# Performance work log

Hardware: AMD Instinct MI355X
Metric: run time of the kernel (lower is better)

## Reference

```python
import jax, jax.numpy as jnp
import numpy as np

B, S, E = 4, 2048, 1024


def setup_inputs() -> dict:
    key = jax.random.key(0)
    k1, k2, k3, k4 = jax.random.split(key, 4)
    scale = 1.0 / np.sqrt(E)
    return {
        "x": jax.random.normal(k1, (B, S, E), dtype=jnp.float32),
        "W_Q": jax.random.normal(k2, (E, E), dtype=jnp.float32) * scale,
        "W_K": jax.random.normal(k3, (E, E), dtype=jnp.float32) * scale,
        "W_V": jax.random.normal(k4, (E, E), dtype=jnp.float32) * scale,
    }


def reference(x, W_Q, W_K, W_V):
    # nn.Linear(E, E, bias=False): y = x @ W.T
    Q = jnp.einsum("bse,fe->bsf", x, W_Q)
    K = jnp.einsum("bse,fe->bsf", x, W_K)
    V = jnp.einsum("bse,fe->bsf", x, W_V)
    d = Q.shape[-1]
    scores = jnp.einsum("bqd,bkd->bqk", Q, K) / jnp.sqrt(jnp.float32(d))
    # causal mask: -inf strictly above the diagonal
    seq = Q.shape[1]
    causal = jnp.tril(jnp.ones((seq, seq), dtype=bool))  # [S,S]
    scores = jnp.where(causal[None, :, :], scores, jnp.float32(-jnp.inf))
    attn = jax.nn.softmax(scores, axis=-1)
    return jnp.einsum("bqk,bkd->bqd", attn, V)
```

## Files before the change

kernel.cpp:

```cpp
#include <hip/hip_runtime.h>
#include <hip/hip_bf16.h>
#include <stdint.h>

typedef __hip_bfloat16 bf16;
typedef __attribute__((ext_vector_type(8))) short bf16x8;
typedef __attribute__((ext_vector_type(4))) float f32x4;
typedef __attribute__((ext_vector_type(8))) unsigned short u16x8;
typedef __attribute__((ext_vector_type(4))) unsigned short u16x4;

#define SLEN 2048
#define ED   1024
#define NB   4
#define AS1 __attribute__((address_space(1)))
#define AS3 __attribute__((address_space(3)))
#define SB0() __builtin_amdgcn_sched_barrier(0)

static __device__ __forceinline__ unsigned short f2bf(float f) {
    return __builtin_bit_cast(unsigned short, __float2bfloat16(f));
}

__device__ __forceinline__ void gemm8p(
    const char* __restrict__ aT, int lda,
    const char* __restrict__ bT, int ldb,
    int nkt, char* sm, int tid, f32x4 (&acc)[8][4])
{
    const int lane = tid & 63, wave = tid >> 6;
    const int wm = wave >> 2, wn = wave & 3;
    const int fr = lane & 15, kc = lane >> 4;

    auto SU = [&](int isB, int kh, int Tn) {
        char* dst = sm + (Tn & 1) * 65536 + isB * 32768 + kh * 16384;
        const char* g = isB ? bT : aT;
        const int ld = isB ? ldb : lda;
#pragma unroll
        for (int j = 0; j < 2; ++j) {
            int rid = j * 512 + tid;
            int row = rid >> 2, c = rid & 3;
            const char* src = g + (size_t)row * ld + Tn * 128 + kh * 64
                            + ((c ^ ((row >> 1) & 3)) * 16);
            __builtin_amdgcn_global_load_lds(
                (const AS1 uint32_t*)src,
                (AS3 uint32_t*)(dst + (j * 512 + wave * 64) * 16), 16, 0, 0);
        }
    };
    auto RDA = [&](int T, int kh, bf16x8 (&a)[8]) {
        const char* pa = sm + (T & 1) * 65536 + kh * 16384;
#pragma unroll
        for (int i = 0; i < 8; ++i) {
            int row = wm * 128 + i * 16 + fr;
            a[i] = *(const bf16x8*)(pa + row * 64 + ((kc ^ ((row >> 1) & 3)) * 16));
        }
    };
    auto RDB = [&](int T, int kh, int nh, bf16x8 (&b)[2]) {
        const char* pb = sm + (T & 1) * 65536 + 32768 + kh * 16384;
#pragma unroll
        for (int n = 0; n < 2; ++n) {
            int row = wn * 64 + nh * 32 + n * 16 + fr;
            b[n] = *(const bf16x8*)(pb + row * 64 + ((kc ^ ((row >> 1) & 3)) * 16));
        }
    };
    auto MM = [&](bf16x8 (&a)[8], bf16x8 (&b)[2], int nh) {
        __builtin_amdgcn_s_setprio(1);
#pragma unroll
        for (int i = 0; i < 8; ++i)
#pragma unroll
            for (int n = 0; n < 2; ++n)
                acc[i][nh * 2 + n] = __builtin_amdgcn_mfma_f32_16x16x32_bf16(
                    a[i], b[n], acc[i][nh * 2 + n], 0, 0, 0);
        __builtin_amdgcn_s_setprio(0);
    };

    SU(0, 0, 0); SU(1, 0, 0); SU(0, 1, 0); SU(1, 1, 0);
    SU(0, 0, 1); SU(1, 0, 1); SU(0, 1, 1);
    asm volatile("s_waitcnt vmcnt(6)" ::: "memory");
    SB0();
    __builtin_amdgcn_s_barrier();

    for (int T = 0; T < nkt; ++T) {
        const bool p1 = (T + 1 < nkt), p2 = (T + 2 < nkt);
        bf16x8 a[8], b[2];
        RDA(T, 0, a); RDB(T, 0, 0, b);
        if (p1) SU(1, 1, T + 1);
        SB0(); __builtin_amdgcn_s_barrier();
        asm volatile("s_waitcnt lgkmcnt(0)" ::: "memory");
        SB0();
        MM(a, b, 0);
        SB0(); __builtin_amdgcn_s_barrier();
        RDB(T, 0, 1, b);
        if (p2) SU(0, 0, T + 2);
        SB0(); __builtin_amdgcn_s_barrier();
        asm volatile("s_waitcnt lgkmcnt(0)" ::: "memory");
        SB0();
        MM(a, b, 1);
        SB0(); __builtin_amdgcn_s_barrier();
        RDA(T, 1, a); RDB(T, 1, 0, b);
        if (p2) SU(1, 0, T + 2);
        SB0(); __builtin_amdgcn_s_barrier();
        asm volatile("s_waitcnt lgkmcnt(0)" ::: "memory");
        SB0();
        MM(a, b, 0);
        SB0(); __builtin_amdgcn_s_barrier();
        RDB(T, 1, 1, b);
        if (p2) SU(0, 1, T + 2);
        if (T < nkt - 2) asm volatile("s_waitcnt vmcnt(6)" ::: "memory");
        else             asm volatile("s_waitcnt vmcnt(0)" ::: "memory");
        SB0(); __builtin_amdgcn_s_barrier();
        asm volatile("s_waitcnt lgkmcnt(0)" ::: "memory");
        SB0();
        MM(a, b, 1);
        SB0(); __builtin_amdgcn_s_barrier();
    }
}

__device__ __forceinline__ void gemm_core8(
    const char* __restrict__ aT, int lda,
    const char* __restrict__ bT, int ldb,
    int nkt, char* sm, int tid, f32x4 (&acc)[4][4])
{
    const int lane = tid & 63, wave = tid >> 6;
    const int wm = wave >> 1, wn = wave & 1;
    const int fr = lane & 15, kc = lane >> 4;

    auto STAGE = [&](int kh, int Tn) {
        char* buf = sm + (Tn & 1) * 49152;
#pragma unroll
        for (int j = 0; j < 2; ++j) {
            int rid = j * 512 + tid;
            int row = rid >> 2, c = rid & 3;
            const char* src = aT + (size_t)row * lda + Tn * 128 + kh * 64
                            + ((c ^ ((row >> 1) & 3)) * 16);
            __builtin_amdgcn_global_load_lds(
                (const AS1 uint32_t*)src,
                (AS3 uint32_t*)(buf + kh * 16384 + (j * 512 + wave * 64) * 16),
                16, 0, 0);
        }
        {
            int row = tid >> 2, c = tid & 3;
            const char* src = bT + (size_t)row * ldb + Tn * 128 + kh * 64
                            + ((c ^ ((row >> 1) & 3)) * 16);
            __builtin_amdgcn_global_load_lds(
                (const AS1 uint32_t*)src,
                (AS3 uint32_t*)(buf + 32768 + kh * 8192 + (wave * 64) * 16),
                16, 0, 0);
        }
    };
    auto RD = [&](int T, int kh, bf16x8 (&a)[4], bf16x8 (&b)[4]) {
        const char* buf = sm + (T & 1) * 49152;
#pragma unroll
        for (int i = 0; i < 4; ++i) {
            int row = wm * 64 + i * 16 + fr;
            a[i] = *(const bf16x8*)(buf + kh * 16384 + row * 64
                                    + ((kc ^ ((row >> 1) & 3)) * 16));
        }
#pragma unroll
        for (int i = 0; i < 4; ++i) {
            int row = wn * 64 + i * 16 + fr;
            b[i] = *(const bf16x8*)(buf + 32768 + kh * 8192 + row * 64
                                    + ((kc ^ ((row >> 1) & 3)) * 16));
        }
    };
    auto MM = [&](bf16x8 (&a)[4], bf16x8 (&b)[4]) {
        __builtin_amdgcn_s_setprio(1);
#pragma unroll
        for (int i = 0; i < 4; ++i)
#pragma unroll
            for (int n = 0; n < 4; ++n)
                acc[i][n] = __builtin_amdgcn_mfma_f32_16x16x32_bf16(
                    a[i], b[n], acc[i][n], 0, 0, 0);
        __builtin_amdgcn_s_setprio(0);
    };

    STAGE(0, 0); STAGE(1, 0);
    asm volatile("s_waitcnt vmcnt(3)" ::: "memory");
    SB0();
    __builtin_amdgcn_s_barrier();

    bf16x8 aE[4], bE[4], aO[4], bO[4];
    for (int T = 0; T < nkt; ++T) {
        const bool pre = (T + 1 < nkt);
        RD(T, 0, aE, bE);
        SB0();
        if (pre) STAGE(0, T + 1);
        SB0();
        if (T > 0) {
            asm volatile("s_waitcnt lgkmcnt(8)" ::: "memory");
            SB0();
            MM(aO, bO);
        }
        if (pre) asm volatile("s_waitcnt vmcnt(3)" ::: "memory");
        else     asm volatile("s_waitcnt vmcnt(0)" ::: "memory");
        SB0();
        __builtin_amdgcn_s_barrier();
        RD(T, 1, aO, bO);
        SB0();
        if (pre) STAGE(1, T + 1);
        SB0();
        asm volatile("s_waitcnt lgkmcnt(8)" ::: "memory");
        SB0();
        MM(aE, bE);
        if (pre) asm volatile("s_waitcnt vmcnt(3)" ::: "memory");
        else     asm volatile("s_waitcnt vmcnt(0)" ::: "memory");
        SB0();
        __builtin_amdgcn_s_barrier();
    }
    asm volatile("s_waitcnt lgkmcnt(0)" ::: "memory");
    SB0();
    MM(aO, bO);
}

__global__ __launch_bounds__(256) void convert_to_bf16(
    const float* __restrict__ x, const float* __restrict__ wq,
    const float* __restrict__ wk, const float* __restrict__ wv,
    bf16* __restrict__ xb, bf16* __restrict__ wqb,
    bf16* __restrict__ wkb, bf16* __restrict__ wvb)
{
    long g = (long)blockIdx.x * 256 + threadIdx.x;
    const float* src; bf16* dst; long o;
    if (g < 1048576) { src = x; dst = xb; o = g * 8; }
    else {
        long g2 = g - 1048576;
        int w = (int)(g2 >> 17);
        o = (g2 & 131071) * 8;
        src = (w == 0) ? wq : (w == 1) ? wk : wv;
        dst = (w == 0) ? wqb : (w == 1) ? wkb : wvb;
    }
    float4 v0 = *(const float4*)(src + o);
    float4 v1 = *(const float4*)(src + o + 4);
    u16x8 r;
    r[0] = f2bf(v0.x); r[1] = f2bf(v0.y); r[2] = f2bf(v0.z); r[3] = f2bf(v0.w);
    r[4] = f2bf(v1.x); r[5] = f2bf(v1.y); r[6] = f2bf(v1.z); r[7] = f2bf(v1.w);
    *(u16x8*)(dst + o) = r;
}

__global__ __launch_bounds__(512, 2) void qkv_gemm(
    const bf16* __restrict__ xb, const bf16* __restrict__ wqb,
    const bf16* __restrict__ wkb, const bf16* __restrict__ wvb,
    bf16* __restrict__ Qb, bf16* __restrict__ Kb, bf16* __restrict__ Vt)
{
    extern __shared__ char smem[];
    int bid = blockIdx.x, tid = threadIdx.x;
    int xcd = bid & 7, i = bid >> 3;
    int tm = (xcd << 2) | (i & 3);
    int tn = i >> 2;
    const bf16* W = (tn < 8) ? wqb : (tn < 16) ? wkb : wvb;
    int tnl = tn & 7;
    f32x4 acc[4][4] = {};
    gemm_core8((const char*)(xb + (size_t)tm * 256 * ED), ED * 2,
               (const char*)(W + (size_t)tnl * 128 * ED), ED * 2,
               16, smem, tid, acc);

    int lane = tid & 63, wave = tid >> 6, wm = wave >> 1, wn = wave & 1;
    int rl = (lane >> 4) * 4, cl = lane & 15;
    if (tn < 16) {
        bf16* C = (tn < 8) ? Qb : Kb;
#pragma unroll
        for (int mf = 0; mf < 4; ++mf)
#pragma unroll
            for (int j = 0; j < 4; ++j) {
                int r = tm * 256 + wm * 64 + mf * 16 + rl + j;
#pragma unroll
                for (int nf = 0; nf < 4; ++nf) {
                    int c = tnl * 128 + wn * 64 + nf * 16 + cl;
                    C[(size_t)r * ED + c] = __float2bfloat16(acc[mf][nf][j]);
                }
            }
    } else {
#pragma unroll
        for (int mf = 0; mf < 4; ++mf)
#pragma unroll
            for (int j = 0; j < 4; ++j) {
                int r = tm * 256 + wm * 64 + mf * 16 + rl + j;
                int bb = r >> 11, s = r & 2047;
#pragma unroll
                for (int nf = 0; nf < 4; ++nf) {
                    int d = tnl * 128 + wn * 64 + nf * 16 + cl;
                    Vt[(((size_t)bb << 10) + d) * SLEN + s] = __float2bfloat16(acc[mf][nf][j]);
                }
            }
    }
}

__global__ __launch_bounds__(512, 2) void qk_gemm(
    const bf16* __restrict__ Qb, const bf16* __restrict__ Kb, float* __restrict__ Sc)
{
    extern __shared__ char smem[];
    int t = blockIdx.x, b = blockIdx.y, tid = threadIdx.x;
    int ti = 0;
    while ((ti + 1) * (ti + 2) / 2 <= t) ++ti;
    int tj = t - ti * (ti + 1) / 2;
    f32x4 acc[8][4] = {};
    gemm8p((const char*)(Qb + ((size_t)b * SLEN + ti * 256) * ED), ED * 2,
           (const char*)(Kb + ((size_t)b * SLEN + tj * 256) * ED), ED * 2,
           16, smem, tid, acc);

    float* Sb = Sc + (size_t)b * SLEN * SLEN;
    int lane = tid & 63, wave = tid >> 6, wm = wave >> 2, wn = wave & 3;
    int rl = (lane >> 4) * 4, cl = lane & 15;
#pragma unroll
    for (int mf = 0; mf < 8; ++mf)
#pragma unroll
        for (int j = 0; j < 4; ++j) {
            int r = ti * 256 + wm * 128 + mf * 16 + rl + j;
#pragma unroll
            for (int nf = 0; nf < 4; ++nf) {
                int c = tj * 256 + wn * 64 + nf * 16 + cl;
                Sb[(size_t)r * SLEN + c] = acc[mf][nf][j] * 0.03125f;
            }
        }
}

__global__ __launch_bounds__(256) void softmax_rows(float* __restrict__ Sc)
{
    int q = blockIdx.x, b = blockIdx.y, tid = threadIdx.x;
    float* row = Sc + ((size_t)b * SLEN + q) * SLEN;
    int lane = tid & 63, wave = tid >> 6;
    __shared__ float red[4];

    float vals[8];
    float lmax = -3.0e38f;
#pragma unroll
    for (int r = 0; r < 2; ++r) {
        int i4 = tid + r * 256;
        if (i4 * 4 <= q) {
            float4 v = *(const float4*)(row + i4 * 4);
            vals[r * 4 + 0] = v.x; vals[r * 4 + 1] = v.y;
            vals[r * 4 + 2] = v.z; vals[r * 4 + 3] = v.w;
#pragma unroll
            for (int e = 0; e < 4; ++e) {
                int k = i4 * 4 + e;
                if (k <= q) lmax = fmaxf(lmax, vals[r * 4 + e]);
            }
        }
    }
#pragma unroll
    for (int o = 32; o > 0; o >>= 1) lmax = fmaxf(lmax, __shfl_xor(lmax, o));
    if (lane == 0) red[wave] = lmax;
    __syncthreads();
    float m = fmaxf(fmaxf(red[0], red[1]), fmaxf(red[2], red[3]));
    __syncthreads();
    float lsum = 0.f;
#pragma unroll
    for (int r = 0; r < 2; ++r) {
        int i4 = tid + r * 256;
        if (i4 * 4 <= q)
#pragma unroll
            for (int e = 0; e < 4; ++e) {
                int k = i4 * 4 + e;
                if (k <= q) lsum += __expf(vals[r * 4 + e] - m);
            }
    }
#pragma unroll
    for (int o = 32; o > 0; o >>= 1) lsum += __shfl_xor(lsum, o);
    if (lane == 0) red[wave] = lsum;
    __syncthreads();
    float inv = 1.0f / (red[0] + red[1] + red[2] + red[3]);
    unsigned short* prow = (unsigned short*)row;
    int kmax = ((q >> 8) + 1) << 8;
#pragma unroll
    for (int r = 0; r < 2; ++r) {
        int i4 = tid + r * 256;
        if (i4 * 4 < kmax) {
            u16x4 o4;
#pragma unroll
            for (int e = 0; e < 4; ++e) {
                int k = i4 * 4 + e;
                float p = (k <= q) ? __expf(vals[r * 4 + e] - m) * inv : 0.0f;
                o4[e] = f2bf(p);
            }
            *(u16x4*)(prow + i4 * 4) = o4;
        }
    }
}

__global__ __launch_bounds__(512, 2) void pv_gemm(
    const bf16* __restrict__ P, const bf16* __restrict__ Vt, float* __restrict__ O)
{
    extern __shared__ char smem[];
    int mq = 7 - blockIdx.x, nd = blockIdx.y, b = blockIdx.z, tid = threadIdx.x;
    f32x4 acc[4][4] = {};
    int nkt = (mq + 1) * 4;
    gemm_core8((const char*)P + ((size_t)b * SLEN + mq * 256) * 8192, 8192,
               (const char*)(Vt + ((size_t)b * ED + nd * 128) * SLEN), SLEN * 2,
               nkt, smem, tid, acc);

    int lane = tid & 63, wave = tid >> 6, wm = wave >> 1, wn = wave & 1;
    int rl = (lane >> 4) * 4, cl = lane & 15;
    float* Ob = O + (size_t)b * SLEN * ED;
#pragma unroll
    for (int mf = 0; mf < 4; ++mf)
#pragma unroll
        for (int j = 0; j < 4; ++j) {
            int r = mq * 256 + wm * 64 + mf * 16 + rl + j;
#pragma unroll
            for (int nf = 0; nf < 4; ++nf) {
                int c = nd * 128 + wn * 64 + nf * 16 + cl;
                Ob[(size_t)r * ED + c] = acc[mf][nf][j];
            }
        }
}

extern "C" void kernel_launch(void* const* d_in, const int* in_sizes, int n_in,
                              void* d_out, int out_size, void* d_ws, size_t ws_size,
                              hipStream_t stream)
{
    const float* x  = (const float*)d_in[0];
    const float* wq = (const float*)d_in[1];
    const float* wk = (const float*)d_in[2];
    const float* wv = (const float*)d_in[3];
    float* out = (float*)d_out;

    char* ws = (char*)d_ws;
    bf16* xb  = (bf16*)(ws);
    bf16* wqb = (bf16*)(ws + 16777216);
    bf16* wkb = (bf16*)(ws + 18874368);
    bf16* wvb = (bf16*)(ws + 20971520);
    bf16* Qb  = (bf16*)(ws + 23068672);
    bf16* Kb  = (bf16*)(ws + 39845888);
    bf16* Vt  = (bf16*)(ws + 56623104);
    float* Sc = (float*)(ws + 73400320);

    (void)hipFuncSetAttribute((const void*)qkv_gemm,
            hipFuncAttributeMaxDynamicSharedMemorySize, 98304);
    (void)hipFuncSetAttribute((const void*)qk_gemm,
            hipFuncAttributeMaxDynamicSharedMemorySize, 131072);
    (void)hipFuncSetAttribute((const void*)pv_gemm,
            hipFuncAttributeMaxDynamicSharedMemorySize, 98304);

    convert_to_bf16<<<5632, 256, 0, stream>>>(x, wq, wk, wv, xb, wqb, wkb, wvb);
    qkv_gemm<<<768, 512, 98304, stream>>>(xb, wqb, wkb, wvb, Qb, Kb, Vt);
    qk_gemm<<<dim3(36, NB), 512, 131072, stream>>>(Qb, Kb, Sc);
    softmax_rows<<<dim3(SLEN, NB), 256, 0, stream>>>(Sc);
    pv_gemm<<<dim3(8, 8, NB), 512, 98304, stream>>>((const bf16*)Sc, Vt, out);
}
```

Before: 153.4 us.

## Split-K the long causal PV row blocks and reorder blocks for load balance

```diff
diff --git a/kernel.cpp b/kernel.cpp
--- a/kernel.cpp
+++ b/kernel.cpp
@@ -373,30 +373,72 @@
 }
 
 __global__ __launch_bounds__(512, 2) void pv_gemm(
-    const bf16* __restrict__ P, const bf16* __restrict__ Vt, float* __restrict__ O)
+    const bf16* __restrict__ P, const bf16* __restrict__ Vt,
+    float* __restrict__ O, float* __restrict__ pp0, float* __restrict__ pp1)
 {
     extern __shared__ char smem[];
-    int mq = 7 - blockIdx.x, nd = blockIdx.y, b = blockIdx.z, tid = threadIdx.x;
+    int g = blockIdx.x, tid = threadIdx.x;
+    int mq, nd, b, h, isHalf;
+    if (g < 64)       { isHalf = 1; mq = 7; int w = g;       h = w & 1; b = (w >> 1) & 3; nd = (w >> 3) & 7; }
+    else if (g < 96)  { isHalf = 0; mq = 3; int w = g - 64;  h = 0;     b = w & 3;        nd = (w >> 2) & 7; }
+    else if (g < 160) { isHalf = 1; mq = 6; int w = g - 96;  h = w & 1; b = (w >> 1) & 3; nd = (w >> 3) & 7; }
+    else if (g < 224) { isHalf = 1; mq = 5; int w = g - 160; h = w & 1; b = (w >> 1) & 3; nd = (w >> 3) & 7; }
+    else if (g < 256) { isHalf = 0; mq = 2; int w = g - 224; h = 0;     b = w & 3;        nd = (w >> 2) & 7; }
+    else if (g < 320) { isHalf = 1; mq = 4; int w = g - 256; h = w & 1; b = (w >> 1) & 3; nd = (w >> 3) & 7; }
+    else if (g < 352) { isHalf = 0; mq = 1; int w = g - 320; h = 0;     b = w & 3;        nd = (w >> 2) & 7; }
+    else              { isHalf = 0; mq = 0; int w = g - 352; h = 0;     b = w & 3;        nd = (w >> 2) & 7; }
+
+    int nkt = isHalf ? (mq + 1) * 2 : (mq + 1) * 4;
+    size_t koff = (size_t)h * (mq + 1) * 128 * 2;
     f32x4 acc[4][4] = {};
-    int nkt = (mq + 1) * 4;
-    gemm_core8((const char*)P + ((size_t)b * SLEN + mq * 256) * 8192, 8192,
-               (const char*)(Vt + ((size_t)b * ED + nd * 128) * SLEN), SLEN * 2,
+    gemm_core8((const char*)P + ((size_t)b * SLEN + mq * 256) * 8192 + koff, 8192,
+               (const char*)(Vt + ((size_t)b * ED + nd * 128) * SLEN) + koff, SLEN * 2,
                nkt, smem, tid, acc);
 
     int lane = tid & 63, wave = tid >> 6, wm = wave >> 1, wn = wave & 1;
     int rl = (lane >> 4) * 4, cl = lane & 15;
-    float* Ob = O + (size_t)b * SLEN * ED;
-#pragma unroll
-    for (int mf = 0; mf < 4; ++mf)
-#pragma unroll
-        for (int j = 0; j < 4; ++j) {
-            int r = mq * 256 + wm * 64 + mf * 16 + rl + j;
-#pragma unroll
-            for (int nf = 0; nf < 4; ++nf) {
-                int c = nd * 128 + wn * 64 + nf * 16 + cl;
-                Ob[(size_t)r * ED + c] = acc[mf][nf][j];
-            }
-        }
+    if (isHalf) {
+        float* pp = h ? pp1 : pp0;
+#pragma unroll
+        for (int mf = 0; mf < 4; ++mf)
+#pragma unroll
+            for (int j = 0; j < 4; ++j) {
+                int r = mq * 256 + wm * 64 + mf * 16 + rl + j;
+#pragma unroll
+                for (int nf = 0; nf < 4; ++nf) {
+                    int c = nd * 128 + wn * 64 + nf * 16 + cl;
+                    pp[(((size_t)b << 10) + (r - 1024)) * ED + c] = acc[mf][nf][j];
+                }
+            }
+    } else {
+        float* Ob = O + (size_t)b * SLEN * ED;
+#pragma unroll
+        for (int mf = 0; mf < 4; ++mf)
+#pragma unroll
+            for (int j = 0; j < 4; ++j) {
+                int r = mq * 256 + wm * 64 + mf * 16 + rl + j;
+#pragma unroll
+                for (int nf = 0; nf < 4; ++nf) {
+                    int c = nd * 128 + wn * 64 + nf * 16 + cl;
+                    Ob[(size_t)r * ED + c] = acc[mf][nf][j];
+                }
+            }
+    }
+}
+
+__global__ __launch_bounds__(256) void reduce_tail(
+    const float* __restrict__ pp0, const float* __restrict__ pp1,
+    float* __restrict__ O)
+{
+    int t = blockIdx.x * 256 + threadIdx.x;
+    int b = t >> 18, rem = t & 262143;
+    const float4* p04 = (const float4*)pp0;
+    const float4* p14 = (const float4*)pp1;
+    float4* O4 = (float4*)O;
+    size_t pi = ((size_t)b << 18) + rem;
+    float4 a = p04[pi], c = p14[pi];
+    O4[((size_t)b * SLEN + 1024) * (ED / 4) + rem] =
+        make_float4(a.x + c.x, a.y + c.y, a.z + c.z, a.w + c.w);
 }
 
 extern "C" void kernel_launch(void* const* d_in, const int* in_sizes, int n_in,
@@ -418,6 +460,8 @@
     bf16* Kb  = (bf16*)(ws + 39845888);
     bf16* Vt  = (bf16*)(ws + 56623104);
     float* Sc = (float*)(ws + 73400320);
+    float* pp0 = (float*)(ws + 23068672);
+    float* pp1 = (float*)(ws + 39845888);
 
     (void)hipFuncSetAttribute((const void*)qkv_gemm,
             hipFuncAttributeMaxDynamicSharedMemorySize, 98304);
@@ -430,5 +474,6 @@
     qkv_gemm<<<768, 512, 98304, stream>>>(xb, wqb, wkb, wvb, Qb, Kb, Vt);
     qk_gemm<<<dim3(36, NB), 512, 131072, stream>>>(Qb, Kb, Sc);
     softmax_rows<<<dim3(SLEN, NB), 256, 0, stream>>>(Sc);
-    pv_gemm<<<dim3(8, 8, NB), 512, 98304, stream>>>((const bf16*)Sc, Vt, out);
-}
+    pv_gemm<<<384, 512, 98304, stream>>>((const bf16*)Sc, Vt, out, pp0, pp1);
+    reduce_tail<<<4096, 256, 0, stream>>>(pp0, pp1, out);
+}
```

New measurement: 153.5 us. Within noise of the previous version (+0.1%).
